# Kernel tuning notes

Measured on AMD Instinct MI355X. Metric: run time of the kernel, lower is better.

## Reference

```python
import jax, jax.numpy as jnp
import numpy as np

D_MODEL = 768
N_HEADS = 12
HEAD_DIM = D_MODEL // N_HEADS
BATCH = 1
SEQ = 4096


def setup_inputs() -> dict:
    key = jax.random.key(0)
    ks = jax.random.split(key, 5)
    std = 1.0 / np.sqrt(D_MODEL)
    return {
        "x": jax.random.normal(ks[0], (BATCH, SEQ, D_MODEL), dtype=jnp.float32),
        "Wq": jax.random.normal(ks[1], (D_MODEL, D_MODEL), dtype=jnp.float32) * std,
        "Wk": jax.random.normal(ks[2], (D_MODEL, D_MODEL), dtype=jnp.float32) * std,
        "Wv": jax.random.normal(ks[3], (D_MODEL, D_MODEL), dtype=jnp.float32) * std,
        "Wp": jax.random.normal(ks[4], (D_MODEL, D_MODEL), dtype=jnp.float32) * std,
    }


def reference(x, Wq, Wk, Wv, Wp):
    B, S, D = x.shape
    scale = HEAD_DIM ** -0.5
    # torch Linear: y = x @ W.T ; reshape to [B, H, S, hd]
    def split_heads(y):
        return y.reshape(B, S, N_HEADS, HEAD_DIM).transpose(0, 2, 1, 3)
    q = split_heads(x @ Wq.T)
    k = split_heads(x @ Wk.T)
    v = split_heads(x @ Wv.T)
    # full [B, H, S, S] scores, as in the original module
    att = jnp.einsum("bhqd,bhkd->bhqk", q, k) * scale
    causal = jnp.tril(jnp.ones((S, S), dtype=bool))
    att = jnp.where(causal[None, None], att, -jnp.inf)
    att = jax.nn.softmax(att, axis=-1)
    y = jnp.einsum("bhqk,bhkd->bhqd", att, v)
    y = y.transpose(0, 2, 1, 3).reshape(B, S, D)
    return y @ Wp.T
```

## Files before the change

kernel.cpp:

```cpp
#include <hip/hip_runtime.h>
#include <hip/hip_bf16.h>
#include <stdint.h>

#define DM 768
#define SQ 4096
#define NH 12

typedef __bf16 bf16;
typedef __bf16 bf16x8 __attribute__((ext_vector_type(8)));
typedef float floatx4 __attribute__((ext_vector_type(4)));
typedef short short4v __attribute__((ext_vector_type(4)));

#if defined(__has_builtin)
#if __has_builtin(__builtin_amdgcn_mfma_f32_16x16x16bf16_1k)
#define HAVE_MFMA16 1
#endif
#endif
#ifndef HAVE_MFMA16
#define HAVE_MFMA16 0
#endif

typedef __attribute__((address_space(1))) const uint32_t cu32_g;
typedef __attribute__((address_space(3))) uint32_t u32_l;

__device__ __forceinline__ uint16_t f2bf(float f) {
  uint32_t u = __builtin_bit_cast(uint32_t, f);
  u += 0x7fff + ((u >> 16) & 1);
  return (uint16_t)(u >> 16);
}

__device__ __forceinline__ uint32_t pk2(float lo, float hi) {
  __hip_bfloat162 h = __float22bfloat162_rn(float2{lo, hi});
  uint32_t u;
  __builtin_memcpy(&u, &h, 4);
  return u;
}

__device__ __forceinline__ float bflo(uint32_t u) {
  return __builtin_bit_cast(float, u << 16);
}
__device__ __forceinline__ float bfhi(uint32_t u) {
  return __builtin_bit_cast(float, u & 0xffff0000u);
}

__device__ __forceinline__ void async16(const bf16* g, bf16* l) {
  __builtin_amdgcn_global_load_lds((cu32_g*)g, (u32_l*)l, 16, 0, 0);
}

__global__ __launch_bounds__(256) void cvt_kernel(
    const float* __restrict__ x, const float* __restrict__ wq,
    const float* __restrict__ wk, const float* __restrict__ wv,
    const float* __restrict__ wp, bf16* __restrict__ xb, bf16* __restrict__ wqb,
    bf16* __restrict__ wkb, bf16* __restrict__ wvb, bf16* __restrict__ wpb) {
  const int XQ = (SQ * DM) / 4;
  const int WQ = (DM * DM) / 4;
  int t = blockIdx.x * 256 + threadIdx.x;
  const float* src;
  bf16* dst;
  int local;
  if (t < XQ) { src = x;  dst = xb;  local = t; }
  else if (t < XQ + WQ)     { src = wq; dst = wqb; local = t - XQ; }
  else if (t < XQ + 2 * WQ) { src = wk; dst = wkb; local = t - XQ - WQ; }
  else if (t < XQ + 3 * WQ) { src = wv; dst = wvb; local = t - XQ - 2 * WQ; }
  else                      { src = wp; dst = wpb; local = t - XQ - 3 * WQ; }
  float4 v = ((const float4*)src)[local];
  ushort4 o;
  o.x = f2bf(v.x); o.y = f2bf(v.y); o.z = f2bf(v.z); o.w = f2bf(v.w);
  ((ushort4*)dst)[local] = o;
}

__device__ __forceinline__ void gemm_core(const bf16* __restrict__ A,
                                          const bf16* __restrict__ B, int m0,
                                          int n0, floatx4 (&acc)[4][4]) {
  __shared__ bf16 lA[128 * 32];
  __shared__ bf16 lB[128 * 32];
  const int tid = threadIdx.x;
  const int lane = tid & 63;
  const int w = tid >> 6;

  const int r0 = w * 32 + (lane >> 2);
  const int ke = (((lane & 3) ^ ((lane >> 3) & 3))) * 8;
  const bf16* gA0 = A + (size_t)(m0 + r0) * DM + ke;
  const bf16* gA1 = A + (size_t)(m0 + r0 + 16) * DM + ke;
  const bf16* gB0 = B + (size_t)(n0 + r0) * DM + ke;
  const bf16* gB1 = B + (size_t)(n0 + r0 + 16) * DM + ke;
  bf16* lA0 = lA + w * 1024;
  bf16* lA1 = lA + w * 1024 + 512;
  bf16* lB0 = lB + w * 1024;
  bf16* lB1 = lB + w * 1024 + 512;

  const int mrow = (w >> 1) * 64 + (lane & 15);
  const int nrow = (w & 1) * 64 + (lane & 15);
  const int cswz = ((lane >> 4) ^ ((lane >> 1) & 3)) * 8;

  for (int kt = 0; kt < DM / 32; ++kt) {
    __syncthreads();
    async16(gA0, lA0); async16(gA1, lA1);
    async16(gB0, lB0); async16(gB1, lB1);
    gA0 += 32; gA1 += 32; gB0 += 32; gB1 += 32;
    __syncthreads();
    bf16x8 a[4], b[4];
#pragma unroll
    for (int mt = 0; mt < 4; ++mt)
      a[mt] = *(const bf16x8*)&lA[(mrow + mt * 16) * 32 + cswz];
#pragma unroll
    for (int nt = 0; nt < 4; ++nt)
      b[nt] = *(const bf16x8*)&lB[(nrow + nt * 16) * 32 + cswz];
#pragma unroll
    for (int mt = 0; mt < 4; ++mt)
#pragma unroll
      for (int nt = 0; nt < 4; ++nt)
        acc[mt][nt] = __builtin_amdgcn_mfma_f32_16x16x32_bf16(
            a[mt], b[nt], acc[mt][nt], 0, 0, 0);
  }
}

__global__ __launch_bounds__(256) void qkv_kernel(
    const bf16* __restrict__ xb, const bf16* __restrict__ wq,
    const bf16* __restrict__ wk, const bf16* __restrict__ wv,
    bf16* __restrict__ Qb, bf16* __restrict__ Kb, bf16* __restrict__ Vtb) {
  const int z = blockIdx.z;
  const bf16* B = (z == 0) ? wq : (z == 1) ? wk : wv;
  const int m0 = blockIdx.x * 128, n0 = blockIdx.y * 128;
  floatx4 acc[4][4] = {};
  gemm_core(xb, B, m0, n0, acc);
  const int lane = threadIdx.x & 63, w = threadIdx.x >> 6;
  const int quad = lane >> 4, ql = lane & 15;
  const float qs = (z == 0) ? 0.18033688011112042f : 1.0f;
  if (z < 2) {
    bf16* C = (z == 0) ? Qb : Kb;
#pragma unroll
    for (int mt = 0; mt < 4; ++mt)
#pragma unroll
      for (int nt = 0; nt < 4; ++nt) {
        int row = m0 + (w >> 1) * 64 + mt * 16 + quad * 4;
        int col = n0 + (w & 1) * 64 + nt * 16 + ql;
#pragma unroll
        for (int r = 0; r < 4; ++r)
          *(uint16_t*)&C[(size_t)(row + r) * DM + col] = f2bf(acc[mt][nt][r] * qs);
      }
  } else {
#pragma unroll
    for (int mt = 0; mt < 4; ++mt)
#pragma unroll
      for (int nt = 0; nt < 4; ++nt) {
        int row = m0 + (w >> 1) * 64 + mt * 16 + quad * 4;
        int col = n0 + (w & 1) * 64 + nt * 16 + ql;
        uint32_t lo = pk2(acc[mt][nt][0], acc[mt][nt][1]);
        uint32_t hi = pk2(acc[mt][nt][2], acc[mt][nt][3]);
        *(uint2*)&Vtb[(size_t)col * SQ + row] = make_uint2(lo, hi);
      }
  }
}

__global__ __launch_bounds__(256) void proj_kernel(
    const bf16* __restrict__ Ob, const bf16* __restrict__ wp,
    float* __restrict__ out) {
  __shared__ bf16 lA[64 * 32];
  __shared__ bf16 lB[128 * 32];
  const int tid = threadIdx.x, lane = tid & 63, w = tid >> 6;
  const int m0 = blockIdx.x * 64, n0 = blockIdx.y * 128;

  const int ke = (((lane & 3) ^ ((lane >> 3) & 3))) * 8;
  const bf16* gA = Ob + (size_t)(m0 + w * 16 + (lane >> 2)) * DM + ke;
  const bf16* gB0 = wp + (size_t)(n0 + w * 32 + (lane >> 2)) * DM + ke;
  const bf16* gB1 = wp + (size_t)(n0 + w * 32 + (lane >> 2) + 16) * DM + ke;
  bf16* lA0 = lA + w * 512;
  bf16* lB0 = lB + w * 1024;
  bf16* lB1 = lB + w * 1024 + 512;

  const int mrow = (w >> 1) * 32 + (lane & 15);
  const int nrow = (w & 1) * 64 + (lane & 15);
  const int cswz = ((lane >> 4) ^ ((lane >> 1) & 3)) * 8;
  floatx4 acc[2][4] = {};

  for (int kt = 0; kt < DM / 32; ++kt) {
    __syncthreads();
    async16(gA, lA0); async16(gB0, lB0); async16(gB1, lB1);
    gA += 32; gB0 += 32; gB1 += 32;
    __syncthreads();
    bf16x8 a[2], b[4];
#pragma unroll
    for (int mt = 0; mt < 2; ++mt)
      a[mt] = *(const bf16x8*)&lA[(mrow + mt * 16) * 32 + cswz];
#pragma unroll
    for (int nt = 0; nt < 4; ++nt)
      b[nt] = *(const bf16x8*)&lB[(nrow + nt * 16) * 32 + cswz];
#pragma unroll
    for (int mt = 0; mt < 2; ++mt)
#pragma unroll
      for (int nt = 0; nt < 4; ++nt)
        acc[mt][nt] = __builtin_amdgcn_mfma_f32_16x16x32_bf16(
            a[mt], b[nt], acc[mt][nt], 0, 0, 0);
  }
  const int quad = lane >> 4, ql = lane & 15;
#pragma unroll
  for (int mt = 0; mt < 2; ++mt)
#pragma unroll
    for (int nt = 0; nt < 4; ++nt) {
      int row = m0 + (w >> 1) * 32 + mt * 16 + quad * 4;
      int col = n0 + (w & 1) * 64 + nt * 16 + ql;
#pragma unroll
      for (int r = 0; r < 4; ++r)
        out[(size_t)(row + r) * DM + col] = acc[mt][nt][r];
    }
}

__global__ __launch_bounds__(256) void attn_kernel(
    const bf16* __restrict__ Qb, const bf16* __restrict__ Kb,
    const bf16* __restrict__ Vtb, uint16_t* __restrict__ OpartB,
    float* __restrict__ Lpart, bf16* __restrict__ Ob) {
#if HAVE_MFMA16
  __shared__ __align__(16) char smem[49152];
#else
  __shared__ __align__(16) char smem[57344];
#endif
  bf16* lK = (bf16*)smem;
  bf16* lV = (bf16*)(smem + 32768);
#if !HAVE_MFMA16
  bf16* lPt = (bf16*)(smem + 49152);
#endif
  const int tid = threadIdx.x, lane = tid & 63, w = tid >> 6;
  const int quad = lane >> 4, ql = lane & 15;

  int b = blockIdx.x;
  int h = b % NH;
  int i = b / NH;
  int qb, c;
  if (i < 32)      { qb = 31 - (i >> 2); c = i & 3; }
  else if (i < 56) { int t2 = i - 32; qb = 23 - t2 / 3; c = t2 % 3; }
  else if (i < 72) { int t2 = i - 56; qb = 15 - (t2 >> 1); c = t2 & 1; }
  else             { qb = 79 - i; c = 0; }
  const int kv0 = c * 1024;
  const int kv_end = min((qb + 1) * 128, kv0 + 1024);
  const int n_it = (kv_end - kv0) >> 7;
  const bool diag = (kv_end == (qb + 1) * 128);

  bf16x8 qf[2][2];
#pragma unroll
  for (int nt = 0; nt < 2; ++nt)
#pragma unroll
    for (int kt = 0; kt < 2; ++kt)
      qf[nt][kt] = *(const bf16x8*)&Qb[(size_t)(qb * 128 + w * 32 + nt * 16 + ql) * DM +
                                       h * 64 + kt * 32 + quad * 8];

  const int src_e = (((lane & 3) ^ ((lane >> 3) & 3))) * 8;
  const bf16* gK[4];
  const bf16* gV4[4];
#pragma unroll
  for (int t = 0; t < 4; ++t) {
    int o = t * 4096 + w * 1024 + lane * 16;
    int cK = o >> 13, rK = (o & 8191) >> 6;
    gK[t] = Kb + (size_t)(kv0 + rK) * DM + h * 64 + cK * 32 + src_e;
    int dV = w * 16 + (lane >> 2);
    gV4[t] = Vtb + (size_t)(h * 64 + dV) * SQ + kv0 + t * 32 + src_e;
  }

#pragma unroll
  for (int t = 0; t < 4; ++t)
    async16(gK[t], (bf16*)((char*)lK + t * 4096 + w * 1024));

  floatx4 o_acc[4][2] = {};
  float l_s[2] = {0.f, 0.f};
  const int cswz = ((lane >> 4) ^ ((lane >> 1) & 3)) * 8;

  for (int j = 0; j < n_it; ++j) {
    __syncthreads();
#pragma unroll
    for (int t = 0; t < 4; ++t) {
      async16(gV4[t], (bf16*)((char*)lV + t * 4096 + w * 1024));
      gV4[t] += 128;
    }
#pragma unroll
    for (int t = 0; t < 4; ++t) {
      gK[t] += 128 * DM;
      async16(gK[t], (bf16*)((char*)lK + ((j + 1) & 1) * 16384 + t * 4096 + w * 1024));
    }

    const bf16* kbuf = lK + (j & 1) * 8192;
    floatx4 s[8][2] = {};
#pragma unroll
    for (int kt = 0; kt < 2; ++kt)
#pragma unroll
      for (int mt = 0; mt < 8; ++mt) {
        bf16x8 a = *(const bf16x8*)&kbuf[kt * 4096 + (mt * 16 + ql) * 32 + cswz];
#pragma unroll
        for (int nt = 0; nt < 2; ++nt)
          s[mt][nt] = __builtin_amdgcn_mfma_f32_16x16x32_bf16(a, qf[nt][kt],
                                                              s[mt][nt], 0, 0, 0);
      }

    if (diag && j == n_it - 1) {
#pragma unroll
      for (int mt = 0; mt < 8; ++mt)
#pragma unroll
        for (int nt = 0; nt < 2; ++nt)
#pragma unroll
          for (int r = 0; r < 4; ++r) {
            int kpos = mt * 16 + quad * 4 + r;
            int qpos = w * 32 + nt * 16 + ql;
            if (kpos > qpos) s[mt][nt][r] = -1e30f;
          }
    }

    uint2 pp[8][2];
#pragma unroll
    for (int nt = 0; nt < 2; ++nt) {
      float tsum[8];
#pragma unroll
      for (int mt = 0; mt < 8; ++mt) {
        float p0 = __builtin_amdgcn_exp2f(s[mt][nt][0]);
        float p1 = __builtin_amdgcn_exp2f(s[mt][nt][1]);
        float p2 = __builtin_amdgcn_exp2f(s[mt][nt][2]);
        float p3 = __builtin_amdgcn_exp2f(s[mt][nt][3]);
        pp[mt][nt] = make_uint2(pk2(p0, p1), pk2(p2, p3));
        tsum[mt] = (p0 + p1) + (p2 + p3);
      }
      l_s[nt] += ((tsum[0] + tsum[1]) + (tsum[2] + tsum[3])) +
                 ((tsum[4] + tsum[5]) + (tsum[6] + tsum[7]));
    }

    asm volatile("s_waitcnt vmcnt(4)" ::: "memory");

#if HAVE_MFMA16
#pragma unroll
    for (int mt = 0; mt < 8; ++mt) {
      short4v bfr[2];
#pragma unroll
      for (int nt = 0; nt < 2; ++nt) {
        union { uint2 u; short4v v; } pb;
        pb.u = pp[mt][nt];
        bfr[nt] = pb.v;
      }
      const char* vbase = (const char*)lV + (mt >> 1) * 4096 +
          ((((mt & 1) * 2 + (quad >> 1)) ^ ((ql >> 1) & 3)) * 16) +
          (quad & 1) * 8;
#pragma unroll
      for (int mtd = 0; mtd < 4; ++mtd) {
        short4v a = *(const short4v*)(vbase + (mtd * 16 + ql) * 64);
#pragma unroll
        for (int nt = 0; nt < 2; ++nt)
          o_acc[mtd][nt] = __builtin_amdgcn_mfma_f32_16x16x16bf16_1k(
              a, bfr[nt], o_acc[mtd][nt], 0, 0, 0);
      }
    }
#else
    bf16* lp = lPt + w * 1024;
#pragma unroll
    for (int ks = 0; ks < 4; ++ks) {
#pragma unroll
      for (int nt = 0; nt < 2; ++nt) {
        int q32 = nt * 16 + ql;
        int key = (q32 >> 1) & 7;
#pragma unroll
        for (int mtp = 0; mtp < 2; ++mtp) {
          int slot = mtp * 4 + quad;
          *(uint2*)((char*)lp + q32 * 64 + ((slot ^ key) * 8)) = pp[2 * ks + mtp][nt];
        }
      }
      bf16x8 bp[2];
#pragma unroll
      for (int nt = 0; nt < 2; ++nt) {
        int q32 = nt * 16 + ql;
        int key = (q32 >> 1) & 7;
        union { uint2 u[2]; bf16x8 v; } pb;
        pb.u[0] = *(uint2*)((char*)lp + q32 * 64 + (((2 * quad) ^ key) * 8));
        pb.u[1] = *(uint2*)((char*)lp + q32 * 64 + (((2 * quad + 1) ^ key) * 8));
        bp[nt] = pb.v;
      }
#pragma unroll
      for (int mtd = 0; mtd < 4; ++mtd) {
        bf16x8 a = *(const bf16x8*)&lV[ks * 2048 + (mtd * 16 + ql) * 32 + cswz];
#pragma unroll
        for (int nt = 0; nt < 2; ++nt)
          o_acc[mtd][nt] = __builtin_amdgcn_mfma_f32_16x16x32_bf16(
              a, bp[nt], o_acc[mtd][nt], 0, 0, 0);
      }
    }
#endif
  }

  float lf[2];
#pragma unroll
  for (int nt = 0; nt < 2; ++nt) {
    float ls = l_s[nt];
    ls += __shfl_xor(ls, 16);
    ls += __shfl_xor(ls, 32);
    lf[nt] = ls;
  }

  if (kv0 == 0 && diag) {
#pragma unroll
    for (int nt = 0; nt < 2; ++nt) {
      float rl = 1.0f / lf[nt];
      int qg = qb * 128 + w * 32 + nt * 16 + ql;
#pragma unroll
      for (int mtd = 0; mtd < 4; ++mtd) {
        uint32_t lo = pk2(o_acc[mtd][nt][0] * rl, o_acc[mtd][nt][1] * rl);
        uint32_t hi = pk2(o_acc[mtd][nt][2] * rl, o_acc[mtd][nt][3] * rl);
        *(uint2*)&Ob[(size_t)qg * DM + h * 64 + mtd * 16 + quad * 4] =
            make_uint2(lo, hi);
      }
    }
  } else {
    const int ps = (h * 32 + qb) * 4 + c;
#pragma unroll
    for (int nt = 0; nt < 2; ++nt) {
      int q = w * 32 + nt * 16 + ql;
      if (quad == 0) Lpart[ps * 128 + q] = lf[nt];
#pragma unroll
      for (int mtd = 0; mtd < 4; ++mtd) {
        uint32_t lo = pk2(o_acc[mtd][nt][0], o_acc[mtd][nt][1]);
        uint32_t hi = pk2(o_acc[mtd][nt][2], o_acc[mtd][nt][3]);
        *(uint2*)&OpartB[(size_t)ps * 8192 + q * 64 + mtd * 16 + quad * 4] =
            make_uint2(lo, hi);
      }
    }
  }
}

__global__ __launch_bounds__(256) void combine_kernel(
    const uint16_t* __restrict__ OpartB, const float* __restrict__ Lpart,
    bf16* __restrict__ Ob) {
  int b = blockIdx.x;
  int h = b % NH, qb = 8 + b / NH;
  int nch = (qb + 8) >> 3;
  int t = threadIdx.x;
  int q = t >> 1, dh = (t & 1) * 32;
  int ps0 = (h * 32 + qb) * 4;

  float acc[32] = {};
  float L = 0.f;
#pragma unroll
  for (int cc = 0; cc < 4; ++cc)
    if (cc < nch) {
      L += Lpart[(ps0 + cc) * 128 + q];
      const uint4* p =
          (const uint4*)(OpartB + (size_t)(ps0 + cc) * 8192 + q * 64 + dh);
#pragma unroll
      for (int g = 0; g < 4; ++g) {
        uint4 u = p[g];
        acc[g * 8 + 0] += bflo(u.x); acc[g * 8 + 1] += bfhi(u.x);
        acc[g * 8 + 2] += bflo(u.y); acc[g * 8 + 3] += bfhi(u.y);
        acc[g * 8 + 4] += bflo(u.z); acc[g * 8 + 5] += bfhi(u.z);
        acc[g * 8 + 6] += bflo(u.w); acc[g * 8 + 7] += bfhi(u.w);
      }
    }
  float rl = 1.0f / L;
  bf16* dst = &Ob[(size_t)(qb * 128 + q) * DM + h * 64 + dh];
#pragma unroll
  for (int g = 0; g < 4; ++g) {
    uint4 u;
    u.x = pk2(acc[g * 8 + 0] * rl, acc[g * 8 + 1] * rl);
    u.y = pk2(acc[g * 8 + 2] * rl, acc[g * 8 + 3] * rl);
    u.z = pk2(acc[g * 8 + 4] * rl, acc[g * 8 + 5] * rl);
    u.w = pk2(acc[g * 8 + 6] * rl, acc[g * 8 + 7] * rl);
    *(uint4*)&dst[g * 8] = u;
  }
}

extern "C" void kernel_launch(void* const* d_in, const int* in_sizes, int n_in,
                              void* d_out, int out_size, void* d_ws,
                              size_t ws_size, hipStream_t stream) {
  const float* x  = (const float*)d_in[0];
  const float* wq = (const float*)d_in[1];
  const float* wk = (const float*)d_in[2];
  const float* wv = (const float*)d_in[3];
  const float* wp = (const float*)d_in[4];
  char* ws = (char*)d_ws;
  float* Lpart = (float*)(ws);
  bf16* xb   = (bf16*)(ws);
  bf16* wqb  = (bf16*)(ws + 6291456);
  bf16* wkb  = (bf16*)(ws + 7471104);
  bf16* wvb  = (bf16*)(ws + 8650752);
  bf16* wpb  = (bf16*)(ws + 9830400);
  bf16* Qb   = (bf16*)(ws + 11010048);
  bf16* Kb   = (bf16*)(ws + 17301504);
  bf16* Vtb  = (bf16*)(ws + 23592960);
  bf16* Ob   = (bf16*)(ws + 29884416);
  uint16_t* OpartB = (uint16_t*)(ws + 36175872);

  cvt_kernel<<<5376, 256, 0, stream>>>(x, wq, wk, wv, wp, xb, wqb, wkb, wvb, wpb);
  qkv_kernel<<<dim3(32, 6, 3), 256, 0, stream>>>(xb, wqb, wkb, wvb, Qb, Kb, Vtb);
  attn_kernel<<<960, 256, 0, stream>>>(Qb, Kb, Vtb, OpartB, Lpart, Ob);
  combine_kernel<<<288, 256, 0, stream>>>(OpartB, Lpart, Ob);
  proj_kernel<<<dim3(64, 6), 256, 0, stream>>>(Ob, wpb, (float*)d_out);
}
```

Baseline: 192.6 us.

## Double-buffer LDS tiles in GEMM, projection and attention K/V loops

Converts the QKV GEMM and output projection K-loops to ping-pong LDS buffers. The next k-slice is prefetched with async global-to-LDS copies while MFMAs consume the current slice, which removes one barrier per iteration. In attention, K and V are both double-buffered and prefetched one block ahead, and the explicit vmcnt wait is removed in favour of the loop-top barrier. This hides load latency behind compute, at the cost of larger LDS footprints. Attention grows from 48 KB to 64 KB, which can cut how many blocks fit on a CU.

```diff
diff --git a/kernel.cpp b/kernel.cpp
--- a/kernel.cpp
+++ b/kernel.cpp
@@ -72,8 +72,8 @@
 __device__ __forceinline__ void gemm_core(const bf16* __restrict__ A,
                                           const bf16* __restrict__ B, int m0,
                                           int n0, floatx4 (&acc)[4][4]) {
-  __shared__ bf16 lA[128 * 32];
-  __shared__ bf16 lB[128 * 32];
+  __shared__ bf16 lA[2 * 4096];
+  __shared__ bf16 lB[2 * 4096];
   const int tid = threadIdx.x;
   const int lane = tid & 63;
   const int w = tid >> 6;
@@ -84,10 +84,10 @@
   const bf16* gA1 = A + (size_t)(m0 + r0 + 16) * DM + ke;
   const bf16* gB0 = B + (size_t)(n0 + r0) * DM + ke;
   const bf16* gB1 = B + (size_t)(n0 + r0 + 16) * DM + ke;
-  bf16* lA0 = lA + w * 1024;
-  bf16* lA1 = lA + w * 1024 + 512;
-  bf16* lB0 = lB + w * 1024;
-  bf16* lB1 = lB + w * 1024 + 512;
+
+  async16(gA0, lA + w * 1024); async16(gA1, lA + w * 1024 + 512);
+  async16(gB0, lB + w * 1024); async16(gB1, lB + w * 1024 + 512);
+  gA0 += 32; gA1 += 32; gB0 += 32; gB1 += 32;
 
   const int mrow = (w >> 1) * 64 + (lane & 15);
   const int nrow = (w & 1) * 64 + (lane & 15);
@@ -95,17 +95,20 @@
 
   for (int kt = 0; kt < DM / 32; ++kt) {
     __syncthreads();
-    async16(gA0, lA0); async16(gA1, lA1);
-    async16(gB0, lB0); async16(gB1, lB1);
-    gA0 += 32; gA1 += 32; gB0 += 32; gB1 += 32;
-    __syncthreads();
+    if (kt + 1 < DM / 32) {
+      const int nb = ((kt + 1) & 1) * 4096;
+      async16(gA0, lA + nb + w * 1024); async16(gA1, lA + nb + w * 1024 + 512);
+      async16(gB0, lB + nb + w * 1024); async16(gB1, lB + nb + w * 1024 + 512);
+      gA0 += 32; gA1 += 32; gB0 += 32; gB1 += 32;
+    }
+    const int cb = (kt & 1) * 4096;
     bf16x8 a[4], b[4];
 #pragma unroll
     for (int mt = 0; mt < 4; ++mt)
-      a[mt] = *(const bf16x8*)&lA[(mrow + mt * 16) * 32 + cswz];
+      a[mt] = *(const bf16x8*)&lA[cb + (mrow + mt * 16) * 32 + cswz];
 #pragma unroll
     for (int nt = 0; nt < 4; ++nt)
-      b[nt] = *(const bf16x8*)&lB[(nrow + nt * 16) * 32 + cswz];
+      b[nt] = *(const bf16x8*)&lB[cb + (nrow + nt * 16) * 32 + cswz];
 #pragma unroll
     for (int mt = 0; mt < 4; ++mt)
 #pragma unroll
@@ -156,8 +159,8 @@
 __global__ __launch_bounds__(256) void proj_kernel(
     const bf16* __restrict__ Ob, const bf16* __restrict__ wp,
     float* __restrict__ out) {
-  __shared__ bf16 lA[64 * 32];
-  __shared__ bf16 lB[128 * 32];
+  __shared__ bf16 lA[2 * 2048];
+  __shared__ bf16 lB[2 * 4096];
   const int tid = threadIdx.x, lane = tid & 63, w = tid >> 6;
   const int m0 = blockIdx.x * 64, n0 = blockIdx.y * 128;
 
@@ -165,9 +168,10 @@
   const bf16* gA = Ob + (size_t)(m0 + w * 16 + (lane >> 2)) * DM + ke;
   const bf16* gB0 = wp + (size_t)(n0 + w * 32 + (lane >> 2)) * DM + ke;
   const bf16* gB1 = wp + (size_t)(n0 + w * 32 + (lane >> 2) + 16) * DM + ke;
-  bf16* lA0 = lA + w * 512;
-  bf16* lB0 = lB + w * 1024;
-  bf16* lB1 = lB + w * 1024 + 512;
+
+  async16(gA, lA + w * 512);
+  async16(gB0, lB + w * 1024); async16(gB1, lB + w * 1024 + 512);
+  gA += 32; gB0 += 32; gB1 += 32;
 
   const int mrow = (w >> 1) * 32 + (lane & 15);
   const int nrow = (w & 1) * 64 + (lane & 15);
@@ -176,16 +180,20 @@
 
   for (int kt = 0; kt < DM / 32; ++kt) {
     __syncthreads();
-    async16(gA, lA0); async16(gB0, lB0); async16(gB1, lB1);
-    gA += 32; gB0 += 32; gB1 += 32;
-    __syncthreads();
+    if (kt + 1 < DM / 32) {
+      const int nbA = ((kt + 1) & 1) * 2048, nbB = ((kt + 1) & 1) * 4096;
+      async16(gA, lA + nbA + w * 512);
+      async16(gB0, lB + nbB + w * 1024); async16(gB1, lB + nbB + w * 1024 + 512);
+      gA += 32; gB0 += 32; gB1 += 32;
+    }
+    const int cbA = (kt & 1) * 2048, cbB = (kt & 1) * 4096;
     bf16x8 a[2], b[4];
 #pragma unroll
     for (int mt = 0; mt < 2; ++mt)
-      a[mt] = *(const bf16x8*)&lA[(mrow + mt * 16) * 32 + cswz];
+      a[mt] = *(const bf16x8*)&lA[cbA + (mrow + mt * 16) * 32 + cswz];
 #pragma unroll
     for (int nt = 0; nt < 4; ++nt)
-      b[nt] = *(const bf16x8*)&lB[(nrow + nt * 16) * 32 + cswz];
+      b[nt] = *(const bf16x8*)&lB[cbB + (nrow + nt * 16) * 32 + cswz];
 #pragma unroll
     for (int mt = 0; mt < 2; ++mt)
 #pragma unroll
@@ -211,14 +219,10 @@
     const bf16* __restrict__ Vtb, uint16_t* __restrict__ OpartB,
     float* __restrict__ Lpart, bf16* __restrict__ Ob) {
 #if HAVE_MFMA16
-  __shared__ __align__(16) char smem[49152];
+  __shared__ __align__(16) char smem[65536];
 #else
-  __shared__ __align__(16) char smem[57344];
-#endif
-  bf16* lK = (bf16*)smem;
-  bf16* lV = (bf16*)(smem + 32768);
-#if !HAVE_MFMA16
-  bf16* lPt = (bf16*)(smem + 49152);
+  __shared__ __align__(16) char smem[73728];
+  bf16* lPt = (bf16*)(smem + 65536);
 #endif
   const int tid = threadIdx.x, lane = tid & 63, w = tid >> 6;
   const int quad = lane >> 4, ql = lane & 15;
@@ -257,8 +261,12 @@
   }
 
 #pragma unroll
-  for (int t = 0; t < 4; ++t)
-    async16(gK[t], (bf16*)((char*)lK + t * 4096 + w * 1024));
+  for (int t = 0; t < 4; ++t) {
+    async16(gK[t], (bf16*)(smem + t * 4096 + w * 1024));
+    async16(gV4[t], (bf16*)(smem + 16384 + t * 4096 + w * 1024));
+    gK[t] += 128 * DM;
+    gV4[t] += 128;
+  }
 
   floatx4 o_acc[4][2] = {};
   float l_s[2] = {0.f, 0.f};
@@ -266,18 +274,20 @@
 
   for (int j = 0; j < n_it; ++j) {
     __syncthreads();
-#pragma unroll
-    for (int t = 0; t < 4; ++t) {
-      async16(gV4[t], (bf16*)((char*)lV + t * 4096 + w * 1024));
-      gV4[t] += 128;
-    }
-#pragma unroll
-    for (int t = 0; t < 4; ++t) {
-      gK[t] += 128 * DM;
-      async16(gK[t], (bf16*)((char*)lK + ((j + 1) & 1) * 16384 + t * 4096 + w * 1024));
-    }
-
-    const bf16* kbuf = lK + (j & 1) * 8192;
+    if (j + 1 < n_it) {
+      char* dst = smem + ((j + 1) & 1) * 32768;
+#pragma unroll
+      for (int t = 0; t < 4; ++t) {
+        async16(gK[t], (bf16*)(dst + t * 4096 + w * 1024));
+        async16(gV4[t], (bf16*)(dst + 16384 + t * 4096 + w * 1024));
+        gK[t] += 128 * DM;
+        gV4[t] += 128;
+      }
+    }
+    const char* cbuf = smem + (j & 1) * 32768;
+    const bf16* kbuf = (const bf16*)cbuf;
+    const char* vbuf = cbuf + 16384;
+
     floatx4 s[8][2] = {};
 #pragma unroll
     for (int kt = 0; kt < 2; ++kt)
@@ -320,8 +330,6 @@
                  ((tsum[4] + tsum[5]) + (tsum[6] + tsum[7]));
     }
 
-    asm volatile("s_waitcnt vmcnt(4)" ::: "memory");
-
 #if HAVE_MFMA16
 #pragma unroll
     for (int mt = 0; mt < 8; ++mt) {
@@ -332,7 +340,7 @@
         pb.u = pp[mt][nt];
         bfr[nt] = pb.v;
       }
-      const char* vbase = (const char*)lV + (mt >> 1) * 4096 +
+      const char* vbase = vbuf + (mt >> 1) * 4096 +
           ((((mt & 1) * 2 + (quad >> 1)) ^ ((ql >> 1) & 3)) * 16) +
           (quad & 1) * 8;
 #pragma unroll
@@ -370,7 +378,8 @@
       }
 #pragma unroll
       for (int mtd = 0; mtd < 4; ++mtd) {
-        bf16x8 a = *(const bf16x8*)&lV[ks * 2048 + (mtd * 16 + ql) * 32 + cswz];
+        bf16x8 a = *(const bf16x8*)((const bf16*)vbuf + ks * 2048 +
+                                    (mtd * 16 + ql) * 32 + cswz);
 #pragma unroll
         for (int nt = 0; nt < 2; ++nt)
           o_acc[mtd][nt] = __builtin_amdgcn_mfma_f32_16x16x32_bf16(
```

Result: faster. 175.9 us (-8.7%).
